# Kernel tuning notes

Hardware: AMD Instinct MI355X
Metric: run time of the kernel (lower is better)

The kernel has to match this reference:

```python
import jax, jax.numpy as jnp
import numpy as np
from jax import lax

B, CIN, COUT, H, W = 8, 64, 64, 128, 128
KH = KW = 3
STRIDE = PAD = DIL = 1
DG = 1
BOUND = 8.0
HOUT = (H + 2 * PAD - (DIL * (KH - 1) + 1)) // STRIDE + 1
WOUT = (W + 2 * PAD - (DIL * (KW - 1) + 1)) // STRIDE + 1
K = KH * KW


def setup_inputs() -> dict:
    key = jax.random.key(0)
    k0, k1, k2, k3 = jax.random.split(key, 4)
    x = jax.random.normal(k0, (B, CIN, H, W), dtype=jnp.float32)
    weight = jax.random.normal(k1, (COUT, CIN, KH, KW), dtype=jnp.float32) * 0.05
    # conv_offset params (zero-init in the original; randomized here to exercise sampling)
    off_w = jax.random.normal(k2, (2 * K * DG, CIN, 3, 3), dtype=jnp.float32) * 0.01
    off_b = jax.random.normal(k3, (2 * K * DG,), dtype=jnp.float32) * 0.1
    return {"x": x, "weight": weight, "off_w": off_w, "off_b": off_b}


def _conv_offset(x, off_w, off_b):
    # 3x3 conv, stride 1, pad 1 -> [B, 2*K*DG, H, W]
    o = lax.conv_general_dilated(x, off_w, (1, 1), [(1, 1), (1, 1)],
                                 dimension_numbers=("NCHW", "OIHW", "NCHW"))
    return o + off_b[None, :, None, None]


def _deform_conv(x, offset, weight):
    Bn, C, Hin, Win = x.shape
    # offset channel layout: per tap k, channel 2k = y-offset, 2k+1 = x-offset (dg=1)
    off = offset.reshape(Bn, K, 2, HOUT, WOUT)
    off_y, off_x = off[:, :, 0], off[:, :, 1]          # [B, K, Ho, Wo]
    tap_y = jnp.repeat(jnp.arange(KH) * DIL, KW).astype(jnp.float32)  # [K]
    tap_x = jnp.tile(jnp.arange(KW) * DIL, KH).astype(jnp.float32)    # [K]
    base_y = (jnp.arange(HOUT) * STRIDE - PAD).astype(jnp.float32)    # [Ho]
    base_x = (jnp.arange(WOUT) * STRIDE - PAD).astype(jnp.float32)    # [Wo]
    sy = off_y + tap_y[None, :, None, None] + base_y[None, None, :, None]  # [B,K,Ho,Wo]
    sx = off_x + tap_x[None, :, None, None] + base_x[None, None, None, :]

    y0f = jnp.floor(sy)
    x0f = jnp.floor(sx)
    ty = sy - y0f
    tx = sx - x0f
    y0 = y0f.astype(jnp.int32)
    x0 = x0f.astype(jnp.int32)

    img = x.reshape(Bn, C, Hin * Win)
    gather = jax.vmap(lambda im, ix: im[:, ix])  # ([C,HW],[K,Ho,Wo]) -> [C,K,Ho,Wo]

    acc = jnp.zeros((Bn, C, K, HOUT, WOUT), dtype=x.dtype)
    for dy in (0, 1):
        for dx in (0, 1):
            yc = y0 + dy
            xc = x0 + dx
            wgt = (ty if dy else 1.0 - ty) * (tx if dx else 1.0 - tx)
            valid = ((yc >= 0) & (yc < Hin) & (xc >= 0) & (xc < Win)).astype(x.dtype)
            idx = jnp.clip(yc, 0, Hin - 1) * Win + jnp.clip(xc, 0, Win - 1)
            acc = acc + (wgt * valid)[:, None] * gather(img, idx)

    # groups == 1: plain weighted accumulate over taps and input channels
    return jnp.einsum("bckhw,ock->bohw", acc, weight.reshape(COUT, CIN, K))


def reference(x, weight, off_w, off_b):
    offset = jnp.clip(_conv_offset(x, off_w, off_b), -BOUND, BOUND)
    return _deform_conv(x, offset, weight)
```

## Files before the change

### kernel.cpp

```cpp
#include <hip/hip_runtime.h>
#include <math.h>

typedef float  f32x4  __attribute__((ext_vector_type(4)));
typedef __bf16 bf16x8 __attribute__((ext_vector_type(8)));

#define HP_     160
#define PITCH_  (HP_*64)
#define BPITCH_ (HP_*HP_*64)

#define SWZ(row, cb) ((row)*128 + ((cb) ^ (((row)&7)<<4)))

#define XP_BYTES   26214400
#define OFFS_BYTES 9437184
#define WTB_BYTES  73728

__device__ __forceinline__ void gl_lds16(const void* g, void* l) {
    __builtin_amdgcn_global_load_lds(
        (const __attribute__((address_space(1))) void*)g,
        (__attribute__((address_space(3))) void*)l, 16, 0, 0);
}

__global__ __launch_bounds__(256) void k_prep(const float* __restrict__ x,
                                              const float* __restrict__ w,
                                              const float* __restrict__ ow,
                                              __bf16* __restrict__ xp,
                                              __bf16* __restrict__ wtb,
                                              __bf16* __restrict__ owt) {
    int gid = blockIdx.x, tid = threadIdx.x;
    if (gid < 2048) {
        __shared__ float tile[64][65];
        int w0 = (gid & 1) * 64, h = (gid >> 1) & 127, b = gid >> 8;
        int lw = tid & 63, cq4 = tid >> 6;
        const float* xb = x + ((size_t)b * 64) * 16384 + (size_t)h * 128;
        #pragma unroll
        for (int it = 0; it < 16; ++it) {
            int c = it * 4 + cq4;
            tile[c][lw] = xb[(size_t)c * 16384 + w0 + lw];
        }
        __syncthreads();
        int p = tid >> 2, q = tid & 3;
        bf16x8 v0, v1;
        #pragma unroll
        for (int j = 0; j < 8; ++j) {
            v0[j] = (__bf16)tile[q * 16 + j][p];
            v1[j] = (__bf16)tile[q * 16 + 8 + j][p];
        }
        __bf16* dst = xp + (size_t)b * BPITCH_ + (size_t)(h + 16) * PITCH_
                         + (size_t)(w0 + p + 16) * 64 + q * 16;
        *(bf16x8*)dst = v0;
        *(bf16x8*)(dst + 8) = v1;
    } else if (gid < 4352) {
        int i = (gid - 2048) * 256 + tid;
        int b, y, xc, cc;
        if (i < 327680) {
            b = i / 40960; int r = i % 40960;
            int row = r / 1280; y = row < 16 ? row : row + 128;
            int xi = r % 1280; xc = xi >> 3; cc = (xi & 7) * 8;
        } else {
            int j = i - 327680;
            b = j / 32768; int r = j % 32768;
            y = 16 + (r >> 8);
            int xi = r & 255; int xcol = xi >> 3;
            xc = xcol < 16 ? xcol : xcol + 128; cc = (xi & 7) * 8;
        }
        bf16x8 z;
        #pragma unroll
        for (int j = 0; j < 8; ++j) z[j] = (__bf16)0.f;
        *(bf16x8*)(xp + (size_t)b * BPITCH_ + (size_t)y * PITCH_ + (size_t)xc * 64 + cc) = z;
    } else {
        int i = (gid - 4352) * 256 + tid;
        if (i < 36864) {
            int c = i & 63, o = (i >> 6) & 63, k = i >> 12;
            wtb[(k << 12) + (o << 6) + (c ^ ((o & 7) << 3))] = (__bf16)w[(o * 64 + c) * 9 + k];
        }
        if (i < 18432) {
            int c = i & 63, o = (i >> 6) & 31, k = i >> 11;
            owt[(k << 11) + (o << 6) + (c ^ ((o & 7) << 3))] =
                (o < 18) ? (__bf16)ow[(o * 64 + c) * 9 + k] : (__bf16)0.f;
        }
    }
}

__global__ __launch_bounds__(256) void k_offconv(const __bf16* __restrict__ xp,
                                                 const __bf16* __restrict__ owt,
                                                 const float* __restrict__ off_b,
                                                 float* __restrict__ offs) {
    __shared__ alignas(16) short wlo[9 * 32 * 64];
    int gid = blockIdx.x, tid = threadIdx.x;
    int w0 = (gid & 1) * 64, h = (gid >> 1) & 127, b = gid >> 8;
    int lane = tid & 63, wv = tid >> 6, l15 = lane & 15, lg = lane >> 4;

    {
        const char* s = (const char*)owt + wv * 9216 + lane * 16;
        char* d = (char*)wlo + wv * 9216;
        #pragma unroll
        for (int it = 0; it < 9; ++it) gl_lds16(s + it * 1024, d + it * 1024);
    }

    f32x4 acc0, acc1;
    #pragma unroll
    for (int r = 0; r < 4; ++r) {
        int o = lg * 4 + r;
        acc0[r] = (o < 18) ? off_b[o] : 0.f;
        acc1[r] = (o + 16 < 18) ? off_b[o + 16] : 0.f;
    }
    __syncthreads();

    int px = wv * 16 + l15;
    const __bf16* pbase = xp + (size_t)b * BPITCH_ + (size_t)(h + 15) * PITCH_
                             + (size_t)(w0 + px + 15) * 64 + lg * 8;
    #pragma unroll
    for (int tap = 0; tap < 9; ++tap) {
        const __bf16* bsrc = pbase + (tap / 3) * PITCH_ + (tap % 3) * 64;
        const char* wb = (const char*)wlo + tap * 4096;
        #pragma unroll
        for (int ks = 0; ks < 2; ++ks) {
            int cb = ks * 64 + lg * 16;
            bf16x8 a0 = *(const bf16x8*)(wb + SWZ(l15, cb));
            bf16x8 a1 = *(const bf16x8*)(wb + SWZ(16 + l15, cb));
            bf16x8 bv = *(const bf16x8*)(bsrc + ks * 32);
            acc0 = __builtin_amdgcn_mfma_f32_16x16x32_bf16(a0, bv, acc0, 0, 0, 0);
            acc1 = __builtin_amdgcn_mfma_f32_16x16x32_bf16(a1, bv, acc1, 0, 0, 0);
        }
    }
    float* obase = offs + (((size_t)b * 128 + h) * 128 + w0 + px) * 18;
    #pragma unroll
    for (int r = 0; r < 4; ++r) {
        int o = lg * 4 + r;
        if (o < 18) obase[o] = fminf(8.f, fmaxf(-8.f, acc0[r]));
        if (o + 16 < 18) obase[o + 16] = fminf(8.f, fmaxf(-8.f, acc1[r]));
    }
}

struct CBank {
    bf16x8 v00a, v00b, v01a, v01b, v10a, v10b, v11a, v11b;
    float ty, tx;
};

__device__ __forceinline__ void load_corners(int tap, CBank& bk,
                                             const float (*offl)[18], int p,
                                             float fh, float fwp,
                                             const __bf16* xb) {
    float2 od = *(const float2*)&offl[p][2 * tap];
    float sy = od.x + (float)(tap / 3) + fh;
    float sx = od.y + (float)(tap % 3) + fwp;
    float yf = floorf(sy), xf = floorf(sx);
    bk.ty = sy - yf; bk.tx = sx - xf;
    int yi = (int)yf, xi = (int)xf;
    const __bf16* s0 = xb + (size_t)(yi * HP_ + xi) * 64;
    bk.v00a = ((const bf16x8*)s0)[0];        bk.v00b = ((const bf16x8*)s0)[1];
    bk.v01a = ((const bf16x8*)(s0 + 64))[0]; bk.v01b = ((const bf16x8*)(s0 + 64))[1];
    const __bf16* s1 = s0 + PITCH_;
    bk.v10a = ((const bf16x8*)s1)[0];        bk.v10b = ((const bf16x8*)s1)[1];
    bk.v11a = ((const bf16x8*)(s1 + 64))[0]; bk.v11b = ((const bf16x8*)(s1 + 64))[1];
}

__device__ __forceinline__ void interp_store(const CBank& bk, char* smb,
                                             int p, int cq) {
    float ty = bk.ty, tx = bk.tx;
    float w00 = (1.f - ty) * (1.f - tx), w01 = (1.f - ty) * tx;
    float w10 = ty * (1.f - tx),         w11 = ty * tx;
    bf16x8 h0, h1;
    #pragma unroll
    for (int j = 0; j < 8; ++j) {
        float r0 = w00 * (float)bk.v00a[j] + w01 * (float)bk.v01a[j]
                 + w10 * (float)bk.v10a[j] + w11 * (float)bk.v11a[j];
        float r1 = w00 * (float)bk.v00b[j] + w01 * (float)bk.v01b[j]
                 + w10 * (float)bk.v10b[j] + w11 * (float)bk.v11b[j];
        h0[j] = (__bf16)r0; h1[j] = (__bf16)r1;
    }
    int cb0 = cq * 32;
    *(bf16x8*)(smb + SWZ(p, cb0))      = h0;
    *(bf16x8*)(smb + SWZ(p, cb0 + 16)) = h1;
}

__global__ __launch_bounds__(256) void k_deform(const __bf16* __restrict__ xp,
                                                const float* __restrict__ offs,
                                                const __bf16* __restrict__ wtb,
                                                float* __restrict__ out) {
    __shared__ alignas(16) short wl[3][4096];
    __shared__ alignas(16) short sm[2][4096];
    __shared__ float offl[64][18];

    int gid = blockIdx.x, tid = threadIdx.x;
    int w0 = (gid & 1) * 64, h = (gid >> 1) & 127, b = gid >> 8;
    int lane = tid & 63, wv = tid >> 6, l15 = lane & 15, lg = lane >> 4;
    int p = tid >> 2, cq = tid & 3;
    int m2 = (wv >> 1) * 2, n2 = (wv & 1) * 2;

    const char* wsrc = (const char*)wtb;
    {
        const char* s = wsrc + wv * 2048 + lane * 16;
        char* d = (char*)wl[0] + wv * 2048;
        gl_lds16(s, d); gl_lds16(s + 1024, d + 1024);
    }
    {
        const float* osrc = offs + (((size_t)b * 128 + h) * 128 + w0) * 18;
        float* od = &offl[0][0];
        #pragma unroll
        for (int it = 0; it < 5; ++it) {
            int i = tid + it * 256;
            if (i < 1152) od[i] = osrc[i];
        }
    }
    __syncthreads();

    const __bf16* xb = xp + (size_t)b * BPITCH_ + cq * 16;
    float fh  = (float)(h - 1 + 16);
    float fwp = (float)(w0 + p - 1 + 16);

    CBank bk0, bk1;
    load_corners(0, bk0, offl, p, fh, fwp, xb);
    {
        const char* s = wsrc + 8192 + wv * 2048 + lane * 16;
        char* d = (char*)wl[1] + wv * 2048;
        gl_lds16(s, d); gl_lds16(s + 1024, d + 1024);
    }
    interp_store(bk0, (char*)sm[0], p, cq);
    load_corners(1, bk1, offl, p, fh, fwp, xb);
    __syncthreads();

    f32x4 acc00, acc01, acc10, acc11;
    #pragma unroll
    for (int r = 0; r < 4; ++r) { acc00[r] = 0.f; acc01[r] = 0.f; acc10[r] = 0.f; acc11[r] = 0.f; }

    #pragma unroll
    for (int k = 0; k < 9; ++k) {
        const char* wb = (const char*)wl[k % 3];
        const char* sb = (const char*)sm[k & 1];
        #pragma unroll
        for (int ks = 0; ks < 2; ++ks) {
            int cb = ks * 64 + lg * 16;
            bf16x8 aA = *(const bf16x8*)(wb + SWZ(m2 * 16 + l15, cb));
            bf16x8 aB = *(const bf16x8*)(wb + SWZ((m2 + 1) * 16 + l15, cb));
            bf16x8 bA = *(const bf16x8*)(sb + SWZ(n2 * 16 + l15, cb));
            bf16x8 bB = *(const bf16x8*)(sb + SWZ((n2 + 1) * 16 + l15, cb));
            acc00 = __builtin_amdgcn_mfma_f32_16x16x32_bf16(aA, bA, acc00, 0, 0, 0);
            acc01 = __builtin_amdgcn_mfma_f32_16x16x32_bf16(aA, bB, acc01, 0, 0, 0);
            acc10 = __builtin_amdgcn_mfma_f32_16x16x32_bf16(aB, bA, acc10, 0, 0, 0);
            acc11 = __builtin_amdgcn_mfma_f32_16x16x32_bf16(aB, bB, acc11, 0, 0, 0);
        }
        if (k < 7) {
            load_corners(k + 2, (k & 1) ? bk1 : bk0, offl, p, fh, fwp, xb);
            const char* s = wsrc + (k + 2) * 8192 + wv * 2048 + lane * 16;
            char* d = (char*)wl[(k + 2) % 3] + wv * 2048;
            gl_lds16(s, d); gl_lds16(s + 1024, d + 1024);
        }
        if (k < 8) {
            interp_store((k & 1) ? bk0 : bk1, (char*)sm[(k + 1) & 1], p, cq);
            __syncthreads();
        }
    }

    #pragma unroll
    for (int mi = 0; mi < 2; ++mi)
        #pragma unroll
        for (int ni = 0; ni < 2; ++ni) {
            f32x4 a = (mi == 0) ? (ni == 0 ? acc00 : acc01)
                                : (ni == 0 ? acc10 : acc11);
            #pragma unroll
            for (int r = 0; r < 4; ++r) {
                int o  = (m2 + mi) * 16 + lg * 4 + r;
                int px = (n2 + ni) * 16 + l15;
                out[((size_t)b * 64 + o) * 16384 + (size_t)h * 128 + w0 + px] = a[r];
            }
        }
}

extern "C" void kernel_launch(void* const* d_in, const int* in_sizes, int n_in,
                              void* d_out, int out_size, void* d_ws, size_t ws_size,
                              hipStream_t stream) {
    const float* x      = (const float*)d_in[0];
    const float* weight = (const float*)d_in[1];
    const float* off_w  = (const float*)d_in[2];
    const float* off_b  = (const float*)d_in[3];
    float* out = (float*)d_out;

    char* ws = (char*)d_ws;
    __bf16* xp  = (__bf16*)ws;
    float*  offs = (float*)(ws + XP_BYTES);
    __bf16* wtb = (__bf16*)(ws + XP_BYTES + OFFS_BYTES);
    __bf16* owt = (__bf16*)(ws + XP_BYTES + OFFS_BYTES + WTB_BYTES);

    k_prep<<<4496, 256, 0, stream>>>(x, weight, off_w, xp, wtb, owt);
    k_offconv<<<2048, 256, 0, stream>>>(xp, owt, off_b, offs);
    k_deform<<<2048, 256, 0, stream>>>(xp, offs, wtb, out);
}
```

Before: 78.40 us.

## Drop LDS staging in offset and deform convs; read weights directly from global

Removes the LDS staging of weights and of interpolated samples in both conv kernels. Each wave now reads its weight fragments straight from global memory and feeds its own bilinear-interpolated pixels into MFMA registers, which eliminates the block-wide barriers and the swizzled shared-memory layout. In the deform kernel each wave now covers all 64 output channels for its 16 pixels with a register double-buffered corner load, and occupancy hints are added via launch bounds. The trade-off is repeated global or L2 weight reads per wave and higher register pressure, in exchange for no LDS traffic and no synchronisation.

New measurement: 190.7 us. 143% more time.

```diff
diff --git a/kernel.cpp b/kernel.cpp
--- a/kernel.cpp
+++ b/kernel.cpp
@@ -8,17 +8,9 @@
 #define PITCH_  (HP_*64)
 #define BPITCH_ (HP_*HP_*64)
 
-#define SWZ(row, cb) ((row)*128 + ((cb) ^ (((row)&7)<<4)))
-
 #define XP_BYTES   26214400
 #define OFFS_BYTES 9437184
 #define WTB_BYTES  73728
-
-__device__ __forceinline__ void gl_lds16(const void* g, void* l) {
-    __builtin_amdgcn_global_load_lds(
-        (const __attribute__((address_space(1))) void*)g,
-        (__attribute__((address_space(3))) void*)l, 16, 0, 0);
-}
 
 __global__ __launch_bounds__(256) void k_prep(const float* __restrict__ x,
                                               const float* __restrict__ w,
@@ -71,31 +63,23 @@
         int i = (gid - 4352) * 256 + tid;
         if (i < 36864) {
             int c = i & 63, o = (i >> 6) & 63, k = i >> 12;
-            wtb[(k << 12) + (o << 6) + (c ^ ((o & 7) << 3))] = (__bf16)w[(o * 64 + c) * 9 + k];
+            wtb[i] = (__bf16)w[(o * 64 + c) * 9 + k];
         }
         if (i < 18432) {
             int c = i & 63, o = (i >> 6) & 31, k = i >> 11;
-            owt[(k << 11) + (o << 6) + (c ^ ((o & 7) << 3))] =
-                (o < 18) ? (__bf16)ow[(o * 64 + c) * 9 + k] : (__bf16)0.f;
-        }
-    }
-}
-
-__global__ __launch_bounds__(256) void k_offconv(const __bf16* __restrict__ xp,
-                                                 const __bf16* __restrict__ owt,
-                                                 const float* __restrict__ off_b,
-                                                 float* __restrict__ offs) {
-    __shared__ alignas(16) short wlo[9 * 32 * 64];
+            owt[i] = (o < 18) ? (__bf16)ow[(o * 64 + c) * 9 + k] : (__bf16)0.f;
+        }
+    }
+}
+
+__global__ __launch_bounds__(256, 4) void k_offconv(const __bf16* __restrict__ xp,
+                                                    const __bf16* __restrict__ owt,
+                                                    const float* __restrict__ off_b,
+                                                    float* __restrict__ offs) {
     int gid = blockIdx.x, tid = threadIdx.x;
     int w0 = (gid & 1) * 64, h = (gid >> 1) & 127, b = gid >> 8;
     int lane = tid & 63, wv = tid >> 6, l15 = lane & 15, lg = lane >> 4;
-
-    {
-        const char* s = (const char*)owt + wv * 9216 + lane * 16;
-        char* d = (char*)wlo + wv * 9216;
-        #pragma unroll
-        for (int it = 0; it < 9; ++it) gl_lds16(s + it * 1024, d + it * 1024);
-    }
+    int px = wv * 16 + l15;
 
     f32x4 acc0, acc1;
     #pragma unroll
@@ -104,25 +88,25 @@
         acc0[r] = (o < 18) ? off_b[o] : 0.f;
         acc1[r] = (o + 16 < 18) ? off_b[o + 16] : 0.f;
     }
-    __syncthreads();
-
-    int px = wv * 16 + l15;
-    const __bf16* pbase = xp + (size_t)b * BPITCH_ + (size_t)(h + 15) * PITCH_
-                             + (size_t)(w0 + px + 15) * 64 + lg * 8;
+
+    const __bf16* pb = xp + (size_t)b * BPITCH_ + (size_t)(h + 15) * PITCH_
+                          + (size_t)(w0 + px + 15) * 64 + lg * 8;
     #pragma unroll
     for (int tap = 0; tap < 9; ++tap) {
-        const __bf16* bsrc = pbase + (tap / 3) * PITCH_ + (tap % 3) * 64;
-        const char* wb = (const char*)wlo + tap * 4096;
-        #pragma unroll
-        for (int ks = 0; ks < 2; ++ks) {
-            int cb = ks * 64 + lg * 16;
-            bf16x8 a0 = *(const bf16x8*)(wb + SWZ(l15, cb));
-            bf16x8 a1 = *(const bf16x8*)(wb + SWZ(16 + l15, cb));
-            bf16x8 bv = *(const bf16x8*)(bsrc + ks * 32);
-            acc0 = __builtin_amdgcn_mfma_f32_16x16x32_bf16(a0, bv, acc0, 0, 0, 0);
-            acc1 = __builtin_amdgcn_mfma_f32_16x16x32_bf16(a1, bv, acc1, 0, 0, 0);
-        }
-    }
+        const __bf16* bs = pb + (tap / 3) * PITCH_ + (tap % 3) * 64;
+        bf16x8 bv0 = *(const bf16x8*)(bs);
+        bf16x8 bv1 = *(const bf16x8*)(bs + 32);
+        const __bf16* ao = owt + tap * 2048 + l15 * 64 + lg * 8;
+        bf16x8 a00 = *(const bf16x8*)(ao);
+        bf16x8 a01 = *(const bf16x8*)(ao + 32);
+        bf16x8 a10 = *(const bf16x8*)(ao + 1024);
+        bf16x8 a11 = *(const bf16x8*)(ao + 1056);
+        acc0 = __builtin_amdgcn_mfma_f32_16x16x32_bf16(a00, bv0, acc0, 0, 0, 0);
+        acc0 = __builtin_amdgcn_mfma_f32_16x16x32_bf16(a01, bv1, acc0, 0, 0, 0);
+        acc1 = __builtin_amdgcn_mfma_f32_16x16x32_bf16(a10, bv0, acc1, 0, 0, 0);
+        acc1 = __builtin_amdgcn_mfma_f32_16x16x32_bf16(a11, bv1, acc1, 0, 0, 0);
+    }
+
     float* obase = offs + (((size_t)b * 128 + h) * 128 + w0 + px) * 18;
     #pragma unroll
     for (int r = 0; r < 4; ++r) {
@@ -132,139 +116,101 @@
     }
 }
 
-struct CBank {
-    bf16x8 v00a, v00b, v01a, v01b, v10a, v10b, v11a, v11b;
-    float ty, tx;
-};
-
-__device__ __forceinline__ void load_corners(int tap, CBank& bk,
-                                             const float (*offl)[18], int p,
-                                             float fh, float fwp,
-                                             const __bf16* xb) {
-    float2 od = *(const float2*)&offl[p][2 * tap];
-    float sy = od.x + (float)(tap / 3) + fh;
-    float sx = od.y + (float)(tap % 3) + fwp;
+struct Bank { bf16x8 c[8]; float ty, tx; };
+
+__device__ __forceinline__ void load_bank(int k, Bank& bk, const float* my_off,
+                                          float fh, float fw,
+                                          const __bf16* xb_lg) {
+    float2 od = *(const float2*)(my_off + 2 * k);
+    float sy = od.x + (float)(k / 3) + fh;
+    float sx = od.y + (float)(k % 3) + fw;
     float yf = floorf(sy), xf = floorf(sx);
     bk.ty = sy - yf; bk.tx = sx - xf;
     int yi = (int)yf, xi = (int)xf;
-    const __bf16* s0 = xb + (size_t)(yi * HP_ + xi) * 64;
-    bk.v00a = ((const bf16x8*)s0)[0];        bk.v00b = ((const bf16x8*)s0)[1];
-    bk.v01a = ((const bf16x8*)(s0 + 64))[0]; bk.v01b = ((const bf16x8*)(s0 + 64))[1];
+    const __bf16* s0 = xb_lg + (yi * HP_ + xi) * 64;
     const __bf16* s1 = s0 + PITCH_;
-    bk.v10a = ((const bf16x8*)s1)[0];        bk.v10b = ((const bf16x8*)s1)[1];
-    bk.v11a = ((const bf16x8*)(s1 + 64))[0]; bk.v11b = ((const bf16x8*)(s1 + 64))[1];
-}
-
-__device__ __forceinline__ void interp_store(const CBank& bk, char* smb,
-                                             int p, int cq) {
+    bk.c[0] = *(const bf16x8*)(s0);
+    bk.c[1] = *(const bf16x8*)(s0 + 32);
+    bk.c[2] = *(const bf16x8*)(s0 + 64);
+    bk.c[3] = *(const bf16x8*)(s0 + 96);
+    bk.c[4] = *(const bf16x8*)(s1);
+    bk.c[5] = *(const bf16x8*)(s1 + 32);
+    bk.c[6] = *(const bf16x8*)(s1 + 64);
+    bk.c[7] = *(const bf16x8*)(s1 + 96);
+}
+
+__device__ __forceinline__ void interp(const Bank& bk, bf16x8& b0, bf16x8& b1) {
     float ty = bk.ty, tx = bk.tx;
     float w00 = (1.f - ty) * (1.f - tx), w01 = (1.f - ty) * tx;
     float w10 = ty * (1.f - tx),         w11 = ty * tx;
-    bf16x8 h0, h1;
     #pragma unroll
     for (int j = 0; j < 8; ++j) {
-        float r0 = w00 * (float)bk.v00a[j] + w01 * (float)bk.v01a[j]
-                 + w10 * (float)bk.v10a[j] + w11 * (float)bk.v11a[j];
-        float r1 = w00 * (float)bk.v00b[j] + w01 * (float)bk.v01b[j]
-                 + w10 * (float)bk.v10b[j] + w11 * (float)bk.v11b[j];
-        h0[j] = (__bf16)r0; h1[j] = (__bf16)r1;
-    }
-    int cb0 = cq * 32;
-    *(bf16x8*)(smb + SWZ(p, cb0))      = h0;
-    *(bf16x8*)(smb + SWZ(p, cb0 + 16)) = h1;
-}
-
-__global__ __launch_bounds__(256) void k_deform(const __bf16* __restrict__ xp,
-                                                const float* __restrict__ offs,
-                                                const __bf16* __restrict__ wtb,
-                                                float* __restrict__ out) {
-    __shared__ alignas(16) short wl[3][4096];
-    __shared__ alignas(16) short sm[2][4096];
-    __shared__ float offl[64][18];
-
+        float r0 = w00 * (float)bk.c[0][j] + w01 * (float)bk.c[2][j]
+                 + w10 * (float)bk.c[4][j] + w11 * (float)bk.c[6][j];
+        float r1 = w00 * (float)bk.c[1][j] + w01 * (float)bk.c[3][j]
+                 + w10 * (float)bk.c[5][j] + w11 * (float)bk.c[7][j];
+        b0[j] = (__bf16)r0;
+        b1[j] = (__bf16)r1;
+    }
+}
+
+__global__ __launch_bounds__(256, 3) void k_deform(const __bf16* __restrict__ xp,
+                                                   const float* __restrict__ offs,
+                                                   const __bf16* __restrict__ wtb,
+                                                   float* __restrict__ out) {
     int gid = blockIdx.x, tid = threadIdx.x;
     int w0 = (gid & 1) * 64, h = (gid >> 1) & 127, b = gid >> 8;
     int lane = tid & 63, wv = tid >> 6, l15 = lane & 15, lg = lane >> 4;
-    int p = tid >> 2, cq = tid & 3;
-    int m2 = (wv >> 1) * 2, n2 = (wv & 1) * 2;
-
-    const char* wsrc = (const char*)wtb;
-    {
-        const char* s = wsrc + wv * 2048 + lane * 16;
-        char* d = (char*)wl[0] + wv * 2048;
-        gl_lds16(s, d); gl_lds16(s + 1024, d + 1024);
-    }
-    {
-        const float* osrc = offs + (((size_t)b * 128 + h) * 128 + w0) * 18;
-        float* od = &offl[0][0];
-        #pragma unroll
-        for (int it = 0; it < 5; ++it) {
-            int i = tid + it * 256;
-            if (i < 1152) od[i] = osrc[i];
-        }
-    }
-    __syncthreads();
-
-    const __bf16* xb = xp + (size_t)b * BPITCH_ + cq * 16;
-    float fh  = (float)(h - 1 + 16);
-    float fwp = (float)(w0 + p - 1 + 16);
-
-    CBank bk0, bk1;
-    load_corners(0, bk0, offl, p, fh, fwp, xb);
-    {
-        const char* s = wsrc + 8192 + wv * 2048 + lane * 16;
-        char* d = (char*)wl[1] + wv * 2048;
-        gl_lds16(s, d); gl_lds16(s + 1024, d + 1024);
-    }
-    interp_store(bk0, (char*)sm[0], p, cq);
-    load_corners(1, bk1, offl, p, fh, fwp, xb);
-    __syncthreads();
-
-    f32x4 acc00, acc01, acc10, acc11;
-    #pragma unroll
-    for (int r = 0; r < 4; ++r) { acc00[r] = 0.f; acc01[r] = 0.f; acc10[r] = 0.f; acc11[r] = 0.f; }
+    int px = wv * 16 + l15;
+
+    const float* my_off = offs + (((size_t)b * 128 + h) * 128 + w0 + px) * 18;
+    const __bf16* xb_lg = xp + (size_t)b * BPITCH_ + lg * 8;
+    float fh = (float)(h + 15);
+    float fw = (float)(w0 + px + 15);
+
+    f32x4 acc[4];
+    #pragma unroll
+    for (int mi = 0; mi < 4; ++mi)
+        #pragma unroll
+        for (int r = 0; r < 4; ++r) acc[mi][r] = 0.f;
+
+    Bank bank[2];
+    load_bank(0, bank[0], my_off, fh, fw, xb_lg);
 
     #pragma unroll
     for (int k = 0; k < 9; ++k) {
-        const char* wb = (const char*)wl[k % 3];
-        const char* sb = (const char*)sm[k & 1];
-        #pragma unroll
-        for (int ks = 0; ks < 2; ++ks) {
-            int cb = ks * 64 + lg * 16;
-            bf16x8 aA = *(const bf16x8*)(wb + SWZ(m2 * 16 + l15, cb));
-            bf16x8 aB = *(const bf16x8*)(wb + SWZ((m2 + 1) * 16 + l15, cb));
-            bf16x8 bA = *(const bf16x8*)(sb + SWZ(n2 * 16 + l15, cb));
-            bf16x8 bB = *(const bf16x8*)(sb + SWZ((n2 + 1) * 16 + l15, cb));
-            acc00 = __builtin_amdgcn_mfma_f32_16x16x32_bf16(aA, bA, acc00, 0, 0, 0);
-            acc01 = __builtin_amdgcn_mfma_f32_16x16x32_bf16(aA, bB, acc01, 0, 0, 0);
-            acc10 = __builtin_amdgcn_mfma_f32_16x16x32_bf16(aB, bA, acc10, 0, 0, 0);
-            acc11 = __builtin_amdgcn_mfma_f32_16x16x32_bf16(aB, bB, acc11, 0, 0, 0);
-        }
-        if (k < 7) {
-            load_corners(k + 2, (k & 1) ? bk1 : bk0, offl, p, fh, fwp, xb);
-            const char* s = wsrc + (k + 2) * 8192 + wv * 2048 + lane * 16;
-            char* d = (char*)wl[(k + 2) % 3] + wv * 2048;
-            gl_lds16(s, d); gl_lds16(s + 1024, d + 1024);
-        }
-        if (k < 8) {
-            interp_store((k & 1) ? bk0 : bk1, (char*)sm[(k + 1) & 1], p, cq);
-            __syncthreads();
-        }
-    }
-
-    #pragma unroll
-    for (int mi = 0; mi < 2; ++mi)
-        #pragma unroll
-        for (int ni = 0; ni < 2; ++ni) {
-            f32x4 a = (mi == 0) ? (ni == 0 ? acc00 : acc01)
-                                : (ni == 0 ? acc10 : acc11);
-            #pragma unroll
-            for (int r = 0; r < 4; ++r) {
-                int o  = (m2 + mi) * 16 + lg * 4 + r;
-                int px = (n2 + ni) * 16 + l15;
-                out[((size_t)b * 64 + o) * 16384 + (size_t)h * 128 + w0 + px] = a[r];
-            }
-        }
+        if (k < 8) load_bank(k + 1, bank[(k + 1) & 1], my_off, fh, fw, xb_lg);
+        bf16x8 b0, b1;
+        interp(bank[k & 1], b0, b1);
+        const __bf16* wa  = wtb + k * 4096 + l15 * 64 + lg * 8;
+        const __bf16* wa2 = wa + 2048;
+        bf16x8 a00 = *(const bf16x8*)(wa);
+        bf16x8 a01 = *(const bf16x8*)(wa + 32);
+        bf16x8 a10 = *(const bf16x8*)(wa + 1024);
+        bf16x8 a11 = *(const bf16x8*)(wa + 1056);
+        bf16x8 a20 = *(const bf16x8*)(wa2);
+        bf16x8 a21 = *(const bf16x8*)(wa2 + 32);
+        bf16x8 a30 = *(const bf16x8*)(wa2 + 1024);
+        bf16x8 a31 = *(const bf16x8*)(wa2 + 1056);
+        acc[0] = __builtin_amdgcn_mfma_f32_16x16x32_bf16(a00, b0, acc[0], 0, 0, 0);
+        acc[0] = __builtin_amdgcn_mfma_f32_16x16x32_bf16(a01, b1, acc[0], 0, 0, 0);
+        acc[1] = __builtin_amdgcn_mfma_f32_16x16x32_bf16(a10, b0, acc[1], 0, 0, 0);
+        acc[1] = __builtin_amdgcn_mfma_f32_16x16x32_bf16(a11, b1, acc[1], 0, 0, 0);
+        acc[2] = __builtin_amdgcn_mfma_f32_16x16x32_bf16(a20, b0, acc[2], 0, 0, 0);
+        acc[2] = __builtin_amdgcn_mfma_f32_16x16x32_bf16(a21, b1, acc[2], 0, 0, 0);
+        acc[3] = __builtin_amdgcn_mfma_f32_16x16x32_bf16(a30, b0, acc[3], 0, 0, 0);
+        acc[3] = __builtin_amdgcn_mfma_f32_16x16x32_bf16(a31, b1, acc[3], 0, 0, 0);
+    }
+
+    #pragma unroll
+    for (int mi = 0; mi < 4; ++mi) {
+        float* ob = out + ((size_t)b * 64 + mi * 16 + lg * 4) * 16384
+                        + (size_t)h * 128 + w0 + px;
+        ob[0]         = acc[mi][0];
+        ob[16384]     = acc[mi][1];
+        ob[32768]     = acc[mi][2];
+        ob[49152]     = acc[mi][3];
+    }
 }
 
 extern "C" void kernel_launch(void* const* d_in, const int* in_sizes, int n_in,
```
